# Optimization experiments

Measured on AMD Instinct MI355X. Metric: run time of the kernel, lower is better.

Reference implementation:

```python
import jax, jax.numpy as jnp
import numpy as np

B, IN_DIM, H1, H2, C = 8192, 1024, 2048, 2048, 1000
E, TOP_K, RH = 8, 2, 512
QB = 127.0
EPS = 1e-5


def _ste_round(x):
    # straight-through estimator round (BitNet-style)
    return x + jax.lax.stop_gradient(jnp.round(x) - x)


def _act_quant(x):
    # per-token absmax 8-bit activation quantization
    s = QB / jnp.clip(jnp.max(jnp.abs(x), axis=-1, keepdims=True), EPS, None)
    return jnp.clip(_ste_round(x * s), -QB, QB) / s


def _weight_quant(w):
    # ternary 1.58b weight quantization, per-tensor mean-abs scale
    s = jnp.clip(jnp.mean(jnp.abs(w)), EPS, None)
    return jnp.clip(_ste_round(w / s), -1.0, 1.0) * s


def _bit_linear(x, w, b):
    return _act_quant(x) @ _weight_quant(w).T + b


def setup_inputs() -> dict:
    key = jax.random.key(0)
    ks = jax.random.split(key, 12)
    def init(k, shape, fan_in):
        return (jax.random.normal(k, shape, dtype=jnp.float32) / np.sqrt(fan_in)).astype(jnp.float32)
    return {
        "x":  jax.random.normal(ks[0], (B, IN_DIM), dtype=jnp.float32),
        "Wr1": init(ks[1], (RH, IN_DIM), IN_DIM),
        "br1": jnp.zeros((RH,), jnp.float32),
        "Wr2": init(ks[2], (E, RH), RH),
        "br2": jnp.zeros((E,), jnp.float32),
        "W1": init(ks[3], (E, H1, IN_DIM), IN_DIM),
        "b1": jnp.zeros((E, H1), jnp.float32),
        "W2": init(ks[4], (E, H2, H1), H1),
        "b2": jnp.zeros((E, H2), jnp.float32),
        "W3": init(ks[5], (E, C, H2), H2),
        "b3": jnp.zeros((E, C), jnp.float32),
    }


def _forward(x, Wr1, br1, Wr2, br2, W1, b1, W2, b2, W3, b3):
    # Router (eval mode: dropout off)
    h = jax.nn.relu(x @ Wr1.T + br1)
    router_probs = jax.nn.softmax(h @ Wr2.T + br2, axis=1)       # [B, E]
    topk_vals, topk_idx = jax.lax.top_k(router_probs, TOP_K)     # [B, K]

    # dense gate matrix: gate[b,e] = sum_k topk_vals[b,k] * (topk_idx[b,k]==e)
    gates = jnp.sum(topk_vals[..., None] * jax.nn.one_hot(topk_idx, E, dtype=x.dtype), axis=1)  # [B, E]

    def expert(w1, c1, w2, c2, w3, c3):
        y = jax.nn.relu(_bit_linear(x, w1, c1))
        y = jax.nn.relu(_bit_linear(y, w2, c2))
        return _bit_linear(y, w3, c3)                             # [B, C]

    out_all = jax.vmap(expert)(W1, b1, W2, b2, W3, b3)            # [E, B, C]
    outputs = jnp.einsum('ebc,be->bc', out_all, gates) / TOP_K    # [B, C]
    load_balancing_loss = jnp.zeros((), x.dtype)                  # eval mode
    return outputs, router_probs, load_balancing_loss


def reference(x, Wr1, br1, Wr2, br2, W1, b1, W2, b2, W3, b3):
    return _forward(x, Wr1, br1, Wr2, br2, W1, b1, W2, b2, W3, b3)
```

## Files before the change

### kernel.cpp

```cpp
#include <hip/hip_runtime.h>
#include <stdint.h>

#define DEV static __device__ __forceinline__

typedef int v4i __attribute__((ext_vector_type(4)));
typedef short v8s __attribute__((ext_vector_type(8)));
typedef float v4f __attribute__((ext_vector_type(4)));
typedef unsigned short u16x8 __attribute__((ext_vector_type(8)));

constexpr int B_T   = 8192;
constexpr int IN_D  = 1024;
constexpr int H1D   = 2048;
constexpr int H2D   = 2048;
constexpr int CDIM  = 1000;
constexpr int NEXP  = 8;
constexpr int RHD   = 512;
constexpr float QBF  = 127.0f;
constexpr float EPSF = 1e-5f;
constexpr int NSLOT = 2 * B_T;
constexpr int MAXT  = 72;
constexpr float GAP_DELTA = 2e-3f;

DEV void load_lds16(const void* g, void* l) {
  __builtin_amdgcn_global_load_lds(
      (const __attribute__((address_space(1))) uint32_t*)(uintptr_t)g,
      (__attribute__((address_space(3))) uint32_t*)(uint32_t)(uintptr_t)l,
      16, 0, 0);
}

DEV uint32_t pack4(float a, float b, float c, float d, float s) {
  int q0 = (int)rintf(a * s); q0 = q0 > 127 ? 127 : (q0 < -127 ? -127 : q0);
  int q1 = (int)rintf(b * s); q1 = q1 > 127 ? 127 : (q1 < -127 ? -127 : q1);
  int q2 = (int)rintf(c * s); q2 = q2 > 127 ? 127 : (q2 < -127 ? -127 : q2);
  int q3 = (int)rintf(d * s); q3 = q3 > 127 ? 127 : (q3 < -127 ? -127 : q3);
  return (uint32_t)(uint8_t)q0 | ((uint32_t)(uint8_t)q1 << 8) |
         ((uint32_t)(uint8_t)q2 << 16) | ((uint32_t)(uint8_t)q3 << 24);
}

DEV uint16_t f2bf(float f) {
  uint32_t u = __float_as_uint(f);
  return (uint16_t)((u + 0x7FFFu + ((u >> 16) & 1u)) >> 16);
}
DEV float bf2f(uint16_t h) { return __uint_as_float((uint32_t)h << 16); }

DEV const float* slice_base(int t, const float* W1, const float* W2, const float* W3,
                            long& n4) {
  const float* W; long perExpert;
  if (t < 8)       { W = W1; perExpert = (long)H1D * IN_D; }
  else if (t < 16) { W = W2; perExpert = (long)H2D * H1D; }
  else             { W = W3; perExpert = (long)CDIM * H2D; }
  n4 = perExpert >> 2;
  return W + (long)(t & 7) * perExpert;
}

__global__ __launch_bounds__(256) void wabs_all(const float* __restrict__ W1,
                                                const float* __restrict__ W2,
                                                const float* __restrict__ W3,
                                                double* __restrict__ partial) {
  const int t = blockIdx.y;
  long n4;
  const float4* base = (const float4*)slice_base(t, W1, W2, W3, n4);
  double s0 = 0.0, s1 = 0.0, s2 = 0.0, s3 = 0.0;
  const long stride4 = 64L * 256L * 4L;
  for (long i4 = ((long)blockIdx.x * 256 + threadIdx.x) * 4; i4 < n4; i4 += stride4) {
    float4 a = base[i4 + 0];
    float4 b = base[i4 + 1];
    float4 c = base[i4 + 2];
    float4 d = base[i4 + 3];
    s0 += (double)fabsf(a.x) + (double)fabsf(a.y) + (double)fabsf(a.z) + (double)fabsf(a.w);
    s1 += (double)fabsf(b.x) + (double)fabsf(b.y) + (double)fabsf(b.z) + (double)fabsf(b.w);
    s2 += (double)fabsf(c.x) + (double)fabsf(c.y) + (double)fabsf(c.z) + (double)fabsf(c.w);
    s3 += (double)fabsf(d.x) + (double)fabsf(d.y) + (double)fabsf(d.z) + (double)fabsf(d.w);
  }
  __shared__ double red[256];
  red[threadIdx.x] = (s0 + s1) + (s2 + s3);
  __syncthreads();
  for (int st = 128; st > 0; st >>= 1) {
    if ((int)threadIdx.x < st) red[threadIdx.x] += red[threadIdx.x + st];
    __syncthreads();
  }
  if (threadIdx.x == 0) partial[(long)t * 64 + blockIdx.x] = red[0];
}

__global__ void finalize_scales(const double* __restrict__ partial, float* __restrict__ swf) {
  int t = threadIdx.x;
  if (t >= 24) return;
  double s = 0.0;
  for (int i = 0; i < 64; ++i) s += partial[t * 64 + i];
  long cnt = (t < 8) ? (long)H1D * IN_D : (t < 16) ? (long)H2D * H1D : (long)CDIM * H2D;
  float mean = (float)(s / (double)cnt);
  swf[t] = fmaxf(mean, EPSF);
}

__global__ __launch_bounds__(256) void wquant_all(const float* __restrict__ W1,
                                                  const float* __restrict__ W2,
                                                  const float* __restrict__ W3,
                                                  int8_t* __restrict__ wq1,
                                                  int8_t* __restrict__ wq2,
                                                  int8_t* __restrict__ wq3,
                                                  const float* __restrict__ swf) {
  const int t = blockIdx.y;
  long n4;
  const float4* base = (const float4*)slice_base(t, W1, W2, W3, n4);
  int8_t* Wq = (t < 8) ? wq1 : (t < 16) ? wq2 : wq3;
  uint32_t* out = (uint32_t*)(Wq) + (long)(t & 7) * n4;
  const float s = swf[t];
  const long stride4 = 64L * 256L * 4L;
  for (long i4 = ((long)blockIdx.x * 256 + threadIdx.x) * 4; i4 < n4; i4 += stride4) {
#pragma unroll
    for (int j = 0; j < 4; ++j) {
      float4 v = base[i4 + j];
      float t0 = fminf(fmaxf(rintf(v.x / s), -1.f), 1.f);
      float t1 = fminf(fmaxf(rintf(v.y / s), -1.f), 1.f);
      float t2 = fminf(fmaxf(rintf(v.z / s), -1.f), 1.f);
      float t3 = fminf(fmaxf(rintf(v.w / s), -1.f), 1.f);
      out[i4 + j] = (uint32_t)(uint8_t)(int8_t)t0 | ((uint32_t)(uint8_t)(int8_t)t1 << 8) |
                    ((uint32_t)(uint8_t)(int8_t)t2 << 16) | ((uint32_t)(uint8_t)(int8_t)t3 << 24);
    }
  }
}

__global__ __launch_bounds__(256) void actquant_split(const float* __restrict__ X,
                                                      int8_t* __restrict__ Xq,
                                                      float* __restrict__ rcp_out,
                                                      uint16_t* __restrict__ xh,
                                                      uint16_t* __restrict__ xl) {
  const int row = blockIdx.x;
  const int tid = threadIdx.x;
  float4 v = ((const float4*)(X + (size_t)row * IN_D))[tid];
  float mx = fmaxf(fmaxf(fabsf(v.x), fabsf(v.y)), fmaxf(fabsf(v.z), fabsf(v.w)));
#pragma unroll
  for (int m = 1; m < 64; m <<= 1) mx = fmaxf(mx, __shfl_xor(mx, m));
  __shared__ float wmax[4];
  const int lane = tid & 63, w = tid >> 6;
  if (lane == 0) wmax[w] = mx;
  __syncthreads();
  mx = fmaxf(fmaxf(wmax[0], wmax[1]), fmaxf(wmax[2], wmax[3]));
  const float M = fmaxf(mx, EPSF);
  const float s = QBF / M;
  ((uint32_t*)(Xq + (size_t)row * IN_D))[tid] = pack4(v.x, v.y, v.z, v.w, s);
  if (tid == 0) rcp_out[row] = M / QBF;
  float f[4] = {v.x, v.y, v.z, v.w};
  ushort4 hh, ll;
  uint16_t h4[4], l4[4];
#pragma unroll
  for (int j = 0; j < 4; ++j) {
    h4[j] = f2bf(f[j]);
    l4[j] = f2bf(f[j] - bf2f(h4[j]));
  }
  hh.x = h4[0]; hh.y = h4[1]; hh.z = h4[2]; hh.w = h4[3];
  ll.x = l4[0]; ll.y = l4[1]; ll.z = l4[2]; ll.w = l4[3];
  ((ushort4*)xh)[(size_t)row * 256 + tid] = hh;
  ((ushort4*)xl)[(size_t)row * 256 + tid] = ll;
}

__global__ __launch_bounds__(256) void split_bf16(const float* __restrict__ src,
                                                  uint16_t* __restrict__ hi,
                                                  uint16_t* __restrict__ lo, long n4) {
  long i = (long)blockIdx.x * 256 + threadIdx.x;
  if (i >= n4) return;
  float4 v = ((const float4*)src)[i];
  float f[4] = {v.x, v.y, v.z, v.w};
  ushort4 hh, ll;
  uint16_t h4[4], l4[4];
#pragma unroll
  for (int j = 0; j < 4; ++j) {
    h4[j] = f2bf(f[j]);
    l4[j] = f2bf(f[j] - bf2f(h4[j]));
  }
  hh.x = h4[0]; hh.y = h4[1]; hh.z = h4[2]; hh.w = h4[3];
  ll.x = l4[0]; ll.y = l4[1]; ll.z = l4[2]; ll.w = l4[3];
  ((ushort4*)hi)[i] = hh;
  ((ushort4*)lo)[i] = ll;
}

__global__ __launch_bounds__(256) void actquant_y(const uint16_t* __restrict__ Y,
                                                  int8_t* __restrict__ Xq,
                                                  float* __restrict__ rcp_out) {
  const int row = blockIdx.x;
  const int tid = threadIdx.x;
  u16x8 v = ((const u16x8*)(Y + (size_t)row * 2048))[tid];
  float f[8];
  float mx = 0.f;
#pragma unroll
  for (int j = 0; j < 8; ++j) {
    f[j] = bf2f(v[j]);
    mx = fmaxf(mx, fabsf(f[j]));
  }
#pragma unroll
  for (int m = 1; m < 64; m <<= 1) mx = fmaxf(mx, __shfl_xor(mx, m));
  __shared__ float wmax[4];
  const int lane = tid & 63, w = tid >> 6;
  if (lane == 0) wmax[w] = mx;
  __syncthreads();
  mx = fmaxf(fmaxf(wmax[0], wmax[1]), fmaxf(wmax[2], wmax[3]));
  const float M = fmaxf(mx, EPSF);
  const float s = QBF / M;
  uint2 o;
  o.x = pack4(f[0], f[1], f[2], f[3], s);
  o.y = pack4(f[4], f[5], f[6], f[7], s);
  ((uint2*)(Xq + (size_t)row * 2048))[tid] = o;
  if (tid == 0) rcp_out[row] = M / QBF;
}

__global__ __launch_bounds__(256, 1) void router_mfma(
    const uint16_t* __restrict__ xh, const uint16_t* __restrict__ xl,
    const uint16_t* __restrict__ wh, const uint16_t* __restrict__ wl,
    const float* __restrict__ br1, float* __restrict__ h) {
  __shared__ __align__(16) int8_t smem[2][65536];
  const int tid = threadIdx.x;
  const int lane = tid & 63, wid = tid >> 6;
  const int wm = wid >> 1, wn = wid & 1;
  const int row0 = blockIdx.x * 128, col0 = blockIdx.y * 128;

  const uint16_t* mats[4] = {xh, xl, wh, wl};
  const int rb[4] = {row0, row0, col0, col0};
  const uint8_t* src[16];
#pragma unroll
  for (int R = 0; R < 4; ++R)
#pragma unroll
    for (int i = 0; i < 4; ++i) {
      int p = i * 256 + tid;
      int r = p >> 3, c = p & 7;
      int cs = c ^ (r & 7);
      src[R * 4 + i] = (const uint8_t*)mats[R] + ((long)(rb[R] + r) * IN_D + cs * 8) * 2;
    }

  v4f acc[4][4] = {};
  auto stage = [&](int buf, int kt) {
#pragma unroll
    for (int R = 0; R < 4; ++R)
#pragma unroll
      for (int i = 0; i < 4; ++i)
        load_lds16(src[R * 4 + i] + kt * 128,
                   &smem[buf][R * 16384 + i * 4096 + wid * 1024]);
  };

  stage(0, 0);
  asm volatile("s_waitcnt vmcnt(0)" ::: "memory");
  __syncthreads();
  int buf = 0;
  for (int kt = 0; kt < 16; ++kt) {
    if (kt + 1 < 16) stage(buf ^ 1, kt + 1);
#pragma unroll
    for (int ks = 0; ks < 2; ++ks) {
      v8s ah[4], al[4], bh[4], bl[4];
#pragma unroll
      for (int m = 0; m < 4; ++m) {
        int r = wm * 64 + m * 16 + (lane & 15);
        int ch = (ks * 4 + (lane >> 4)) ^ (r & 7);
        ah[m] = *(const v8s*)&smem[buf][r * 128 + ch * 16];
        al[m] = *(const v8s*)&smem[buf][16384 + r * 128 + ch * 16];
      }
#pragma unroll
      for (int n = 0; n < 4; ++n) {
        int r = wn * 64 + n * 16 + (lane & 15);
        int ch = (ks * 4 + (lane >> 4)) ^ (r & 7);
        bh[n] = *(const v8s*)&smem[buf][32768 + r * 128 + ch * 16];
        bl[n] = *(const v8s*)&smem[buf][49152 + r * 128 + ch * 16];
      }
#pragma unroll
      for (int m = 0; m < 4; ++m)
#pragma unroll
        for (int n = 0; n < 4; ++n) {
          acc[m][n] = __builtin_amdgcn_mfma_f32_16x16x32_bf16(ah[m], bh[n], acc[m][n], 0, 0, 0);
          acc[m][n] = __builtin_amdgcn_mfma_f32_16x16x32_bf16(ah[m], bl[n], acc[m][n], 0, 0, 0);
          acc[m][n] = __builtin_amdgcn_mfma_f32_16x16x32_bf16(al[m], bh[n], acc[m][n], 0, 0, 0);
        }
    }
    asm volatile("s_waitcnt vmcnt(0)" ::: "memory");
    __syncthreads();
    buf ^= 1;
  }

  const int rbase = (lane >> 4) * 4;
  const int cfr = lane & 15;
#pragma unroll
  for (int m = 0; m < 4; ++m)
#pragma unroll
    for (int rg = 0; rg < 4; ++rg) {
      int row = row0 + wm * 64 + m * 16 + rbase + rg;
#pragma unroll
      for (int n = 0; n < 4; ++n) {
        int col = col0 + wn * 64 + n * 16 + cfr;
        h[(long)row * RHD + col] = fmaxf(acc[m][n][rg] + br1[col], 0.f);
      }
    }
}

__global__ __launch_bounds__(256) void router_stage2(const float* __restrict__ h,
                                                     const float* __restrict__ Wr2,
                                                     const float* __restrict__ br2,
                                                     float* __restrict__ probs,
                                                     int* __restrict__ idxg,
                                                     float* __restrict__ gvg,
                                                     int* __restrict__ scount,
                                                     int* __restrict__ suspects) {
  __shared__ float w2s[NEXP * RHD];
  const int tid = threadIdx.x;
  for (int i = tid; i < NEXP * RHD; i += 256) w2s[i] = Wr2[i];
  __syncthreads();
  const int lane = tid & 63, w = tid >> 6;
  const int b = blockIdx.x * 4 + w;
  const float* hrow = h + (long)b * RHD;
  float4 v0 = *(const float4*)&hrow[lane * 8];
  float4 v1 = *(const float4*)&hrow[lane * 8 + 4];
  float hr[8] = {v0.x, v0.y, v0.z, v0.w, v1.x, v1.y, v1.z, v1.w};
  float lg[8];
#pragma unroll
  for (int e = 0; e < 8; ++e) {
    float p = 0.f;
#pragma unroll
    for (int j = 0; j < 8; ++j) p = fmaf(hr[j], w2s[e * RHD + lane * 8 + j], p);
#pragma unroll
    for (int m = 1; m < 64; m <<= 1) p += __shfl_xor(p, m);
    lg[e] = p + br2[e];
  }
  if (lane == 0) {
    float mx = lg[0];
#pragma unroll
    for (int e = 1; e < 8; ++e) mx = fmaxf(mx, lg[e]);
    float ex[8], sum = 0.f;
#pragma unroll
    for (int e = 0; e < 8; ++e) { ex[e] = expf(lg[e] - mx); sum += ex[e]; }
#pragma unroll
    for (int e = 0; e < 8; ++e) probs[(long)b * 8 + e] = ex[e] / sum;
    int i0 = 0; float b0 = lg[0];
#pragma unroll
    for (int e = 1; e < 8; ++e) if (lg[e] > b0) { b0 = lg[e]; i0 = e; }
    int i1 = -1; float b1v = -3.4e38f;
#pragma unroll
    for (int e = 0; e < 8; ++e) if (e != i0 && lg[e] > b1v) { b1v = lg[e]; i1 = e; }
    float b2v = -3.4e38f;
#pragma unroll
    for (int e = 0; e < 8; ++e) if (e != i0 && e != i1 && lg[e] > b2v) b2v = lg[e];
    idxg[b * 2 + 0] = i0; idxg[b * 2 + 1] = i1;
    gvg[b * 2 + 0] = ex[i0] / sum; gvg[b * 2 + 1] = ex[i1] / sum;
    if (b1v - b2v < GAP_DELTA) {
      int p = atomicAdd(scount, 1);
      if (p < B_T) suspects[p] = b;
    }
  }
}

__global__ __launch_bounds__(256) void router_fixup(const float* __restrict__ x,
                                                    const float* __restrict__ Wr1,
                                                    const float* __restrict__ br1,
                                                    const float* __restrict__ Wr2,
                                                    const float* __restrict__ br2,
                                                    const int* __restrict__ suspects,
                                                    const int* __restrict__ scount,
                                                    float* __restrict__ probs,
                                                    int* __restrict__ idxg,
                                                    float* __restrict__ gvg) {
  __shared__ float xr[IN_D];
  __shared__ float hr[RHD];
  __shared__ float lgs[NEXP];
  const int n = *scount;
  const int tid = threadIdx.x;
  for (int s = blockIdx.x; s < n && s < B_T; s += 128) {
    const int b = suspects[s];
    __syncthreads();
    for (int i = tid; i < IN_D; i += 256) xr[i] = x[(long)b * IN_D + i];
    __syncthreads();
    {
      const int c0 = tid * 2, c1 = tid * 2 + 1;
      const float* w0 = Wr1 + (long)c0 * IN_D;
      const float* w1 = Wr1 + (long)c1 * IN_D;
      float a0 = 0.f, a1 = 0.f;
      for (int k = 0; k < IN_D; ++k) {
        float xv = xr[k];
        a0 = fmaf(xv, w0[k], a0);
        a1 = fmaf(xv, w1[k], a1);
      }
      hr[c0] = fmaxf(a0 + br1[c0], 0.f);
      hr[c1] = fmaxf(a1 + br1[c1], 0.f);
    }
    __syncthreads();
    if (tid < NEXP) {
      const float* w2 = Wr2 + (long)tid * RHD;
      float a = 0.f;
      for (int k = 0; k < RHD; ++k) a = fmaf(hr[k], w2[k], a);
      lgs[tid] = a + br2[tid];
    }
    __syncthreads();
    if (tid == 0) {
      float lg[8];
#pragma unroll
      for (int e = 0; e < 8; ++e) lg[e] = lgs[e];
      float mx = lg[0];
#pragma unroll
      for (int e = 1; e < 8; ++e) mx = fmaxf(mx, lg[e]);
      float ex[8], sum = 0.f;
#pragma unroll
      for (int e = 0; e < 8; ++e) { ex[e] = expf(lg[e] - mx); sum += ex[e]; }
#pragma unroll
      for (int e = 0; e < 8; ++e) probs[(long)b * 8 + e] = ex[e] / sum;
      int i0 = 0; float b0 = lg[0];
#pragma unroll
      for (int e = 1; e < 8; ++e) if (lg[e] > b0) { b0 = lg[e]; i0 = e; }
      int i1 = -1; float b1v = -3.4e38f;
#pragma unroll
      for (int e = 0; e < 8; ++e) if (e != i0 && lg[e] > b1v) { b1v = lg[e]; i1 = e; }
      idxg[b * 2 + 0] = i0; idxg[b * 2 + 1] = i1;
      gvg[b * 2 + 0] = ex[i0] / sum; gvg[b * 2 + 1] = ex[i1] / sum;
    }
  }
}

__global__ __launch_bounds__(256) void hist_block(const int* __restrict__ idxg,
                                                  int* __restrict__ bc) {
  __shared__ int hloc[NEXP];
  const int t = threadIdx.x;
  if (t < NEXP) hloc[t] = 0;
  __syncthreads();
  int a = blockIdx.x * 256 + t;
  atomicAdd(&hloc[idxg[a]], 1);
  __syncthreads();
  if (t < NEXP) bc[blockIdx.x * NEXP + t] = hloc[t];
}

__global__ void scan_all(const int* __restrict__ bc, int* __restrict__ blockbase,
                         int* __restrict__ ntiles, int* __restrict__ te,
                         int* __restrict__ ts, int* __restrict__ tc,
                         float* __restrict__ loss_out) {
  __shared__ int counts[NEXP], basep[NEXP];
  const int t = threadIdx.x;
  if (t < NEXP) {
    int s = 0;
    for (int b = 0; b < 64; ++b) s += bc[b * NEXP + t];
    counts[t] = s;
  }
  __syncthreads();
  if (t == 0) {
    int acc = 0, nb = 0;
    for (int e = 0; e < NEXP; ++e) {
      basep[e] = acc;
      int c = counts[e];
      int nt = (c + 255) >> 8;
      for (int i = 0; i < nt; ++i) {
        te[nb] = e; ts[nb] = acc + i * 256; tc[nb] = min(256, c - i * 256); ++nb;
      }
      acc += c;
    }
    *ntiles = nb;
    *loss_out = 0.f;
  }
  __syncthreads();
  if (t < NEXP) {
    int run = basep[t];
    for (int b = 0; b < 64; ++b) { blockbase[b * NEXP + t] = run; run += bc[b * NEXP + t]; }
  }
}

__global__ __launch_bounds__(256) void place2(const int* __restrict__ idxg,
                                              const int* __restrict__ blockbase,
                                              int* __restrict__ token_list,
                                              int* __restrict__ slotmap) {
  __shared__ int cur[NEXP];
  const int t = threadIdx.x;
  if (t < NEXP) cur[t] = blockbase[blockIdx.x * NEXP + t];
  __syncthreads();
  int a = blockIdx.x * 256 + t;
  int e = idxg[a];
  int pos = atomicAdd(&cur[e], 1);
  token_list[pos] = a >> 1;
  slotmap[a] = pos;
}

template <int KDIM, bool INDIRECT, bool RELU, bool FINAL>
__global__ __launch_bounds__(512, 2) void gemm_i8(
    const int8_t* __restrict__ Aq, const int8_t* __restrict__ Wq,
    const float* __restrict__ swf_layer, const float* __restrict__ rcp_act,
    const float* __restrict__ bias, const int* __restrict__ te,
    const int* __restrict__ ts, const int* __restrict__ tc,
    const int* __restrict__ ntiles_p, const int* __restrict__ token_list,
    void* __restrict__ Yout, int Nvalid) {
  if ((int)blockIdx.y >= *ntiles_p) return;
  extern __shared__ __align__(16) int8_t smem_dyn[];
  const int t = blockIdx.y;
  const int e = te[t], row0 = ts[t], rcount = tc[t];
  const int col0 = blockIdx.x * 256;
  const int tid = threadIdx.x;
  const int lane = tid & 63, wid = tid >> 6;
  const int wsm = wid >> 2, wsn = wid & 3;
  const int fr = lane & 15, hi = lane >> 4;

  const int8_t* sA[2][2];
  const int8_t* sB[2][2];
#pragma unroll
  for (int hh = 0; hh < 2; ++hh)
#pragma unroll
    for (int i = 0; i < 2; ++i) {
      int p = i * 512 + tid;
      int rl = p >> 3, c = p & 7;
      int cs = c ^ (rl & 7);
      int rt = hh * 128 + rl;
      int ar = row0 + min(rt, rcount - 1);
      long arow = INDIRECT ? (long)token_list[ar] : (long)ar;
      sA[hh][i] = Aq + arow * KDIM + cs * 16;
      int br = min(col0 + rt, Nvalid - 1);
      sB[hh][i] = Wq + ((long)e * Nvalid + br) * (long)KDIM + cs * 16;
    }

  auto stage = [&](int buf, int kt, int which) {
    const int hh = which & 1;
    const bool isB = which >= 2;
    const int8_t* p0 = isB ? sB[hh][0] : sA[hh][0];
    const int8_t* p1 = isB ? sB[hh][1] : sA[hh][1];
    int base = buf * 65536 + (isB ? 32768 : 0) + hh * 16384 + wid * 1024;
    load_lds16(p0 + (long)kt * 128, &smem_dyn[base]);
    load_lds16(p1 + (long)kt * 128, &smem_dyn[base + 8192]);
  };

  const int swz0 = ((0 * 4 + hi) ^ (fr & 7)) * 16 + fr * 128;
  const int swz1 = ((1 * 4 + hi) ^ (fr & 7)) * 16 + fr * 128;

  v4i acc[2][2][4][2] = {};
  v4i aF[4][2];
  v4i bF[2][2][2];

  constexpr int KT = KDIM / 128;
  stage(0, 0, 0); stage(0, 0, 1); stage(0, 0, 2); stage(0, 0, 3);
  stage(1, 1, 0); stage(1, 1, 2); stage(1, 1, 1);
  asm volatile("s_waitcnt vmcnt(6)" ::: "memory");
  asm volatile("s_barrier" ::: "memory");

  for (int kt = 0; kt < KT; ++kt) {
    const int buf = kt & 1;
    const int ab = buf * 65536;
    const int bb = ab + 32768;
#pragma unroll
    for (int mi = 0; mi < 4; ++mi) {
      aF[mi][0] = *(const v4i*)&smem_dyn[ab + (wsm * 64 + mi * 16) * 128 + swz0];
      aF[mi][1] = *(const v4i*)&smem_dyn[ab + (wsm * 64 + mi * 16) * 128 + swz1];
    }
#pragma unroll
    for (int ni = 0; ni < 2; ++ni) {
      bF[0][ni][0] = *(const v4i*)&smem_dyn[bb + (wsn * 32 + ni * 16) * 128 + swz0];
      bF[0][ni][1] = *(const v4i*)&smem_dyn[bb + (wsn * 32 + ni * 16) * 128 + swz1];
    }
    if (kt + 1 < KT) stage(buf ^ 1, kt + 1, 3);
    __builtin_amdgcn_s_setprio(1);
#pragma unroll
    for (int mi = 0; mi < 4; ++mi)
#pragma unroll
      for (int ni = 0; ni < 2; ++ni) {
        acc[0][0][mi][ni] = __builtin_amdgcn_mfma_i32_16x16x64_i8(aF[mi][0], bF[0][ni][0], acc[0][0][mi][ni], 0, 0, 0);
        acc[0][0][mi][ni] = __builtin_amdgcn_mfma_i32_16x16x64_i8(aF[mi][1], bF[0][ni][1], acc[0][0][mi][ni], 0, 0, 0);
      }
    __builtin_amdgcn_s_setprio(0);
    asm volatile("s_barrier" ::: "memory");
#pragma unroll
    for (int ni = 0; ni < 2; ++ni) {
      bF[1][ni][0] = *(const v4i*)&smem_dyn[bb + (128 + wsn * 32 + ni * 16) * 128 + swz0];
      bF[1][ni][1] = *(const v4i*)&smem_dyn[bb + (128 + wsn * 32 + ni * 16) * 128 + swz1];
    }
    if (kt + 2 < KT) stage(buf, kt + 2, 0);
    __builtin_amdgcn_s_setprio(1);
#pragma unroll
    for (int mi = 0; mi < 4; ++mi)
#pragma unroll
      for (int ni = 0; ni < 2; ++ni) {
        acc[0][1][mi][ni] = __builtin_amdgcn_mfma_i32_16x16x64_i8(aF[mi][0], bF[1][ni][0], acc[0][1][mi][ni], 0, 0, 0);
        acc[0][1][mi][ni] = __builtin_amdgcn_mfma_i32_16x16x64_i8(aF[mi][1], bF[1][ni][1], acc[0][1][mi][ni], 0, 0, 0);
      }
    __builtin_amdgcn_s_setprio(0);
    asm volatile("s_barrier" ::: "memory");
#pragma unroll
    for (int mi = 0; mi < 4; ++mi) {
      aF[mi][0] = *(const v4i*)&smem_dyn[ab + (128 + wsm * 64 + mi * 16) * 128 + swz0];
      aF[mi][1] = *(const v4i*)&smem_dyn[ab + (128 + wsm * 64 + mi * 16) * 128 + swz1];
    }
    if (kt + 2 < KT) stage(buf, kt + 2, 2);
    __builtin_amdgcn_s_setprio(1);
#pragma unroll
    for (int mi = 0; mi < 4; ++mi)
#pragma unroll
      for (int ni = 0; ni < 2; ++ni) {
        acc[1][0][mi][ni] = __builtin_amdgcn_mfma_i32_16x16x64_i8(aF[mi][0], bF[0][ni][0], acc[1][0][mi][ni], 0, 0, 0);
        acc[1][0][mi][ni] = __builtin_amdgcn_mfma_i32_16x16x64_i8(aF[mi][1], bF[0][ni][1], acc[1][0][mi][ni], 0, 0, 0);
      }
    __builtin_amdgcn_s_setprio(0);
    asm volatile("s_barrier" ::: "memory");
    if (kt + 2 < KT) stage(buf, kt + 2, 1);
    __builtin_amdgcn_s_setprio(1);
#pragma unroll
    for (int mi = 0; mi < 4; ++mi)
#pragma unroll
      for (int ni = 0; ni < 2; ++ni) {
        acc[1][1][mi][ni] = __builtin_amdgcn_mfma_i32_16x16x64_i8(aF[mi][0], bF[1][ni][0], acc[1][1][mi][ni], 0, 0, 0);
        acc[1][1][mi][ni] = __builtin_amdgcn_mfma_i32_16x16x64_i8(aF[mi][1], bF[1][ni][1], acc[1][1][mi][ni], 0, 0, 0);
      }
    __builtin_amdgcn_s_setprio(0);
    if (kt < KT - 3) {
      asm volatile("s_waitcnt vmcnt(6)" ::: "memory");
    } else {
      asm volatile("s_waitcnt vmcnt(0)" ::: "memory");
    }
    asm volatile("s_barrier" ::: "memory");
  }

  const float sw = swf_layer[e];
  const int rbase = hi * 4;
  const float* bias_e = bias + (long)e * Nvalid;
#pragma unroll
  for (int qm = 0; qm < 2; ++qm)
#pragma unroll
    for (int mi = 0; mi < 4; ++mi)
#pragma unroll
      for (int rg = 0; rg < 4; ++rg) {
        int trow = qm * 128 + wsm * 64 + mi * 16 + rbase + rg;
        if (trow >= rcount) continue;
        int slot = row0 + trow;
        float rcp = rcp_act[INDIRECT ? token_list[slot] : slot];
        float dq = sw * rcp;
        if constexpr (!FINAL) {
          uint16_t* yrow = (uint16_t*)Yout + (long)slot * 2048;
#pragma unroll
          for (int qn = 0; qn < 2; ++qn)
#pragma unroll
            for (int ni = 0; ni < 2; ++ni) {
              int o = col0 + qn * 128 + wsn * 32 + ni * 16 + fr;
              float v = (float)acc[qm][qn][mi][ni][rg] * dq + bias_e[o];
              if (RELU) v = fmaxf(v, 0.f);
              yrow[o] = f2bf(v);
            }
        } else {
          float* zrow = (float*)Yout + (long)slot * 1024;
#pragma unroll
          for (int qn = 0; qn < 2; ++qn)
#pragma unroll
            for (int ni = 0; ni < 2; ++ni) {
              int o = col0 + qn * 128 + wsn * 32 + ni * 16 + fr;
              float bb2 = bias_e[min(o, Nvalid - 1)];
              zrow[o] = (float)acc[qm][qn][mi][ni][rg] * dq + bb2;
            }
        }
      }
}

__global__ __launch_bounds__(256) void combine(const float* __restrict__ z,
                                               const int* __restrict__ slotmap,
                                               const float* __restrict__ gvg,
                                               float* __restrict__ out) {
  const int b = blockIdx.x;
  const int c = threadIdx.x;
  if (c >= 250) return;
  const int s0 = slotmap[b * 2], s1 = slotmap[b * 2 + 1];
  const float g0 = gvg[b * 2] * 0.5f, g1 = gvg[b * 2 + 1] * 0.5f;
  float4 a = *(const float4*)(z + (long)s0 * 1024 + c * 4);
  float4 q = *(const float4*)(z + (long)s1 * 1024 + c * 4);
  float4 o = {g0 * a.x + g1 * q.x, g0 * a.y + g1 * q.y,
              g0 * a.z + g1 * q.z, g0 * a.w + g1 * q.w};
  *(float4*)(out + (long)b * CDIM + c * 4) = o;
}

extern "C" void kernel_launch(void* const* d_in, const int* in_sizes, int n_in,
                              void* d_out, int out_size, void* d_ws, size_t ws_size,
                              hipStream_t stream) {
  const float* x   = (const float*)d_in[0];
  const float* Wr1 = (const float*)d_in[1];
  const float* br1 = (const float*)d_in[2];
  const float* Wr2 = (const float*)d_in[3];
  const float* br2 = (const float*)d_in[4];
  const float* W1  = (const float*)d_in[5];
  const float* b1  = (const float*)d_in[6];
  const float* W2  = (const float*)d_in[7];
  const float* b2  = (const float*)d_in[8];
  const float* W3  = (const float*)d_in[9];
  const float* b3  = (const float*)d_in[10];
  float* out = (float*)d_out;
  char* ws = (char*)d_ws;

  size_t off = 0;
  auto alloc = [&](size_t sz) { size_t r = off; off = (off + sz + 255) & ~(size_t)255; return r; };
  size_t O_META  = alloc(8192);
  size_t O_SUSP  = alloc(B_T * sizeof(int));
  size_t O_PART  = alloc(24 * 64 * sizeof(double));
  size_t O_SWF   = alloc(24 * sizeof(float));
  size_t O_RCPX  = alloc(B_T * sizeof(float));
  size_t O_IDX   = alloc(B_T * 2 * sizeof(int));
  size_t O_GVG   = alloc(B_T * 2 * sizeof(float));
  size_t O_TLIST = alloc(NSLOT * sizeof(int));
  size_t O_SLOT  = alloc(B_T * 2 * sizeof(int));
  size_t O_S1    = alloc(NSLOT * sizeof(float));
  size_t O_S2    = alloc(NSLOT * sizeof(float));
  size_t O_XQ    = alloc((size_t)B_T * IN_D);
  size_t O_WQ1   = alloc((size_t)NEXP * H1D * IN_D);
  size_t O_WQ2   = alloc((size_t)NEXP * H2D * H1D);
  size_t O_WQ3   = alloc((size_t)NEXP * CDIM * H2D);
  size_t O_YQ    = alloc((size_t)NSLOT * 2048);
  size_t O_YBIG  = alloc((size_t)NSLOT * 2048 * sizeof(float));
  (void)ws_size; (void)in_sizes; (void)n_in;

  int*    te     = (int*)(ws + O_META);
  int*    tsv    = te + 144;
  int*    tcv    = tsv + 144;
  int*    ntiles = tcv + 144;
  int*    bc     = ntiles + 4;
  int*    bbase  = bc + 512;
  int*    scount = bbase + 512;
  int*    susp   = (int*)(ws + O_SUSP);
  double* part   = (double*)(ws + O_PART);
  float*  swf    = (float*)(ws + O_SWF);
  float*  rcpx   = (float*)(ws + O_RCPX);
  int*    idxg   = (int*)(ws + O_IDX);
  float*  gvg    = (float*)(ws + O_GVG);
  int*    tlist  = (int*)(ws + O_TLIST);
  int*    slotmap= (int*)(ws + O_SLOT);
  float*  s1     = (float*)(ws + O_S1);
  float*  s2     = (float*)(ws + O_S2);
  int8_t* Xq     = (int8_t*)(ws + O_XQ);
  int8_t* wq1    = (int8_t*)(ws + O_WQ1);
  int8_t* wq2    = (int8_t*)(ws + O_WQ2);
  int8_t* wq3    = (int8_t*)(ws + O_WQ3);
  float*  Ybig   = (float*)(ws + O_YBIG);
  float*  h      = Ybig;
  uint16_t* ybf  = (uint16_t*)Ybig;
  float*  zbuf   = Ybig;
  int8_t* Yq     = (int8_t*)(ws + O_YQ);

  char* ybytes = (char*)Ybig;
  uint16_t* xh = (uint16_t*)(ybytes + (80l << 20));
  uint16_t* xl = (uint16_t*)(ybytes + (97l << 20));
  uint16_t* wh = (uint16_t*)(ybytes + (114l << 20));
  uint16_t* wl = (uint16_t*)(ybytes + (116l << 20));

  hipMemsetAsync(ws + O_META, 0, 8192, stream);

  wabs_all<<<dim3(64, 24), 256, 0, stream>>>(W1, W2, W3, part);
  finalize_scales<<<1, 64, 0, stream>>>(part, swf);
  wquant_all<<<dim3(64, 24), 256, 0, stream>>>(W1, W2, W3, wq1, wq2, wq3, swf);

  actquant_split<<<B_T, 256, 0, stream>>>(x, Xq, rcpx, xh, xl);
  split_bf16<<<512, 256, 0, stream>>>(Wr1, wh, wl, (long)RHD * IN_D / 4);

  router_mfma<<<dim3(B_T / 128, RHD / 128), 256, 0, stream>>>(xh, xl, wh, wl, br1, h);
  router_stage2<<<B_T / 4, 256, 0, stream>>>(h, Wr2, br2, out + (size_t)B_T * CDIM,
                                             idxg, gvg, scount, susp);
  router_fixup<<<128, 256, 0, stream>>>(x, Wr1, br1, Wr2, br2, susp, scount,
                                        out + (size_t)B_T * CDIM, idxg, gvg);
  hist_block<<<64, 256, 0, stream>>>(idxg, bc);
  scan_all<<<1, 64, 0, stream>>>(bc, bbase, ntiles, te, tsv, tcv,
                                 out + (size_t)B_T * CDIM + (size_t)B_T * NEXP);
  place2<<<64, 256, 0, stream>>>(idxg, bbase, tlist, slotmap);

  gemm_i8<IN_D, true, true, false><<<dim3(H1D / 256, MAXT), 512, 131072, stream>>>(
      Xq, wq1, swf + 0, rcpx, b1, te, tsv, tcv, ntiles, tlist, (void*)ybf, H1D);
  actquant_y<<<NSLOT, 256, 0, stream>>>(ybf, Yq, s1);
  gemm_i8<2048, false, true, false><<<dim3(H2D / 256, MAXT), 512, 131072, stream>>>(
      Yq, wq2, swf + 8, s1, b2, te, tsv, tcv, ntiles, tlist, (void*)ybf, H2D);
  actquant_y<<<NSLOT, 256, 0, stream>>>(ybf, Yq, s2);
  gemm_i8<2048, false, false, true><<<dim3(1024 / 256, MAXT), 512, 131072, stream>>>(
      Yq, wq3, swf + 16, s2, b3, te, tsv, tcv, ntiles, tlist, (void*)zbuf, CDIM);

  combine<<<B_T, 256, 0, stream>>>(zbuf, slotmap, gvg, out);
}
```

Measured before the change: 565.8 us.

## Halve GEMM K-tile to 64 and restructure pipeline for higher occupancy

The int8 MFMA GEMM now uses a K step of 64 instead of 128, with a new swizzle and a single 16-byte load per thread per stage. This halves LDS use to 64KB per block and raises launch bounds to allow 4 blocks per CU, aiming to hide latency through occupancy. The prefetch schedule changes from loading two K tiles ahead to one tile ahead, with mid-iteration waits. The cost is twice as many iterations and barriers per unit of K and a shallower prefetch, and the tighter register budget may cause spills.

```diff
diff --git a/kernel.cpp b/kernel.cpp
--- a/kernel.cpp
+++ b/kernel.cpp
@@ -469,7 +469,7 @@
 }
 
 template <int KDIM, bool INDIRECT, bool RELU, bool FINAL>
-__global__ __launch_bounds__(512, 2) void gemm_i8(
+__global__ __launch_bounds__(512, 4) void gemm_i8(
     const int8_t* __restrict__ Aq, const int8_t* __restrict__ Wq,
     const float* __restrict__ swf_layer, const float* __restrict__ rcp_act,
     const float* __restrict__ bias, const int* __restrict__ te,
@@ -486,119 +486,95 @@
   const int wsm = wid >> 2, wsn = wid & 3;
   const int fr = lane & 15, hi = lane >> 4;
 
-  const int8_t* sA[2][2];
-  const int8_t* sB[2][2];
-#pragma unroll
-  for (int hh = 0; hh < 2; ++hh)
-#pragma unroll
-    for (int i = 0; i < 2; ++i) {
-      int p = i * 512 + tid;
-      int rl = p >> 3, c = p & 7;
-      int cs = c ^ (rl & 7);
-      int rt = hh * 128 + rl;
+  const int8_t* sA[2];
+  const int8_t* sB[2];
+  {
+    int r = tid >> 2, c = tid & 3;
+    int cs = c ^ ((r >> 1) & 3);
+#pragma unroll
+    for (int hh = 0; hh < 2; ++hh) {
+      int rt = hh * 128 + r;
       int ar = row0 + min(rt, rcount - 1);
       long arow = INDIRECT ? (long)token_list[ar] : (long)ar;
-      sA[hh][i] = Aq + arow * KDIM + cs * 16;
+      sA[hh] = Aq + arow * KDIM + cs * 16;
       int br = min(col0 + rt, Nvalid - 1);
-      sB[hh][i] = Wq + ((long)e * Nvalid + br) * (long)KDIM + cs * 16;
-    }
+      sB[hh] = Wq + ((long)e * Nvalid + br) * (long)KDIM + cs * 16;
+    }
+  }
 
   auto stage = [&](int buf, int kt, int which) {
     const int hh = which & 1;
-    const bool isB = which >= 2;
-    const int8_t* p0 = isB ? sB[hh][0] : sA[hh][0];
-    const int8_t* p1 = isB ? sB[hh][1] : sA[hh][1];
-    int base = buf * 65536 + (isB ? 32768 : 0) + hh * 16384 + wid * 1024;
-    load_lds16(p0 + (long)kt * 128, &smem_dyn[base]);
-    load_lds16(p1 + (long)kt * 128, &smem_dyn[base + 8192]);
+    const int8_t* p = (which >= 2) ? sB[hh] : sA[hh];
+    int dst = buf * 32768 + (which & 1) * 8192 + ((which >> 1) & 1) * 16384 + wid * 1024;
+    load_lds16(p + (long)kt * 64, &smem_dyn[dst]);
   };
 
-  const int swz0 = ((0 * 4 + hi) ^ (fr & 7)) * 16 + fr * 128;
-  const int swz1 = ((1 * 4 + hi) ^ (fr & 7)) * 16 + fr * 128;
+  const int swzc = (hi ^ ((fr >> 1) & 3)) * 16 + fr * 64;
 
   v4i acc[2][2][4][2] = {};
-  v4i aF[4][2];
-  v4i bF[2][2][2];
-
-  constexpr int KT = KDIM / 128;
-  stage(0, 0, 0); stage(0, 0, 1); stage(0, 0, 2); stage(0, 0, 3);
-  stage(1, 1, 0); stage(1, 1, 2); stage(1, 1, 1);
-  asm volatile("s_waitcnt vmcnt(6)" ::: "memory");
-  asm volatile("s_barrier" ::: "memory");
+  v4i aF[4];
+  v4i bF[2][2];
+
+  constexpr int KT = KDIM / 64;
+  stage(0, 0, 3); stage(0, 0, 0); stage(0, 0, 2); stage(0, 0, 1);
 
   for (int kt = 0; kt < KT; ++kt) {
     const int buf = kt & 1;
-    const int ab = buf * 65536;
-    const int bb = ab + 32768;
-#pragma unroll
-    for (int mi = 0; mi < 4; ++mi) {
-      aF[mi][0] = *(const v4i*)&smem_dyn[ab + (wsm * 64 + mi * 16) * 128 + swz0];
-      aF[mi][1] = *(const v4i*)&smem_dyn[ab + (wsm * 64 + mi * 16) * 128 + swz1];
-    }
-#pragma unroll
-    for (int ni = 0; ni < 2; ++ni) {
-      bF[0][ni][0] = *(const v4i*)&smem_dyn[bb + (wsn * 32 + ni * 16) * 128 + swz0];
-      bF[0][ni][1] = *(const v4i*)&smem_dyn[bb + (wsn * 32 + ni * 16) * 128 + swz1];
-    }
+    const int base = buf * 32768;
+    asm volatile("s_waitcnt vmcnt(1)" ::: "memory");
+    asm volatile("s_barrier" ::: "memory");
+#pragma unroll
+    for (int mi = 0; mi < 4; ++mi)
+      aF[mi] = *(const v4i*)&smem_dyn[base + (wsm * 64 + mi * 16) * 64 + swzc];
+#pragma unroll
+    for (int ni = 0; ni < 2; ++ni)
+      bF[0][ni] = *(const v4i*)&smem_dyn[base + 16384 + (wsn * 32 + ni * 16) * 64 + swzc];
     if (kt + 1 < KT) stage(buf ^ 1, kt + 1, 3);
     __builtin_amdgcn_s_setprio(1);
 #pragma unroll
     for (int mi = 0; mi < 4; ++mi)
 #pragma unroll
-      for (int ni = 0; ni < 2; ++ni) {
-        acc[0][0][mi][ni] = __builtin_amdgcn_mfma_i32_16x16x64_i8(aF[mi][0], bF[0][ni][0], acc[0][0][mi][ni], 0, 0, 0);
-        acc[0][0][mi][ni] = __builtin_amdgcn_mfma_i32_16x16x64_i8(aF[mi][1], bF[0][ni][1], acc[0][0][mi][ni], 0, 0, 0);
-      }
+      for (int ni = 0; ni < 2; ++ni)
+        acc[0][0][mi][ni] = __builtin_amdgcn_mfma_i32_16x16x64_i8(aF[mi], bF[0][ni], acc[0][0][mi][ni], 0, 0, 0);
     __builtin_amdgcn_s_setprio(0);
     asm volatile("s_barrier" ::: "memory");
 #pragma unroll
-    for (int ni = 0; ni < 2; ++ni) {
-      bF[1][ni][0] = *(const v4i*)&smem_dyn[bb + (128 + wsn * 32 + ni * 16) * 128 + swz0];
-      bF[1][ni][1] = *(const v4i*)&smem_dyn[bb + (128 + wsn * 32 + ni * 16) * 128 + swz1];
-    }
-    if (kt + 2 < KT) stage(buf, kt + 2, 0);
+    for (int ni = 0; ni < 2; ++ni)
+      bF[1][ni] = *(const v4i*)&smem_dyn[base + 24576 + (wsn * 32 + ni * 16) * 64 + swzc];
+    if (kt + 1 < KT) stage(buf ^ 1, kt + 1, 0);
     __builtin_amdgcn_s_setprio(1);
 #pragma unroll
     for (int mi = 0; mi < 4; ++mi)
 #pragma unroll
-      for (int ni = 0; ni < 2; ++ni) {
-        acc[0][1][mi][ni] = __builtin_amdgcn_mfma_i32_16x16x64_i8(aF[mi][0], bF[1][ni][0], acc[0][1][mi][ni], 0, 0, 0);
-        acc[0][1][mi][ni] = __builtin_amdgcn_mfma_i32_16x16x64_i8(aF[mi][1], bF[1][ni][1], acc[0][1][mi][ni], 0, 0, 0);
-      }
+      for (int ni = 0; ni < 2; ++ni)
+        acc[0][1][mi][ni] = __builtin_amdgcn_mfma_i32_16x16x64_i8(aF[mi], bF[1][ni], acc[0][1][mi][ni], 0, 0, 0);
+    __builtin_amdgcn_s_setprio(0);
+    if (kt + 1 < KT) {
+      asm volatile("s_waitcnt vmcnt(2)" ::: "memory");
+    } else {
+      asm volatile("s_waitcnt vmcnt(0)" ::: "memory");
+    }
+    asm volatile("s_barrier" ::: "memory");
+#pragma unroll
+    for (int mi = 0; mi < 4; ++mi)
+      aF[mi] = *(const v4i*)&smem_dyn[base + 8192 + (wsm * 64 + mi * 16) * 64 + swzc];
+    if (kt + 1 < KT) stage(buf ^ 1, kt + 1, 2);
+    __builtin_amdgcn_s_setprio(1);
+#pragma unroll
+    for (int mi = 0; mi < 4; ++mi)
+#pragma unroll
+      for (int ni = 0; ni < 2; ++ni)
+        acc[1][0][mi][ni] = __builtin_amdgcn_mfma_i32_16x16x64_i8(aF[mi], bF[0][ni], acc[1][0][mi][ni], 0, 0, 0);
     __builtin_amdgcn_s_setprio(0);
     asm volatile("s_barrier" ::: "memory");
-#pragma unroll
-    for (int mi = 0; mi < 4; ++mi) {
-      aF[mi][0] = *(const v4i*)&smem_dyn[ab + (128 + wsm * 64 + mi * 16) * 128 + swz0];
-      aF[mi][1] = *(const v4i*)&smem_dyn[ab + (128 + wsm * 64 + mi * 16) * 128 + swz1];
-    }
-    if (kt + 2 < KT) stage(buf, kt + 2, 2);
+    if (kt + 1 < KT) stage(buf ^ 1, kt + 1, 1);
     __builtin_amdgcn_s_setprio(1);
 #pragma unroll
     for (int mi = 0; mi < 4; ++mi)
 #pragma unroll
-      for (int ni = 0; ni < 2; ++ni) {
-        acc[1][0][mi][ni] = __builtin_amdgcn_mfma_i32_16x16x64_i8(aF[mi][0], bF[0][ni][0], acc[1][0][mi][ni], 0, 0, 0);
-        acc[1][0][mi][ni] = __builtin_amdgcn_mfma_i32_16x16x64_i8(aF[mi][1], bF[0][ni][1], acc[1][0][mi][ni], 0, 0, 0);
-      }
+      for (int ni = 0; ni < 2; ++ni)
+        acc[1][1][mi][ni] = __builtin_amdgcn_mfma_i32_16x16x64_i8(aF[mi], bF[1][ni], acc[1][1][mi][ni], 0, 0, 0);
     __builtin_amdgcn_s_setprio(0);
-    asm volatile("s_barrier" ::: "memory");
-    if (kt + 2 < KT) stage(buf, kt + 2, 1);
-    __builtin_amdgcn_s_setprio(1);
-#pragma unroll
-    for (int mi = 0; mi < 4; ++mi)
-#pragma unroll
-      for (int ni = 0; ni < 2; ++ni) {
-        acc[1][1][mi][ni] = __builtin_amdgcn_mfma_i32_16x16x64_i8(aF[mi][0], bF[1][ni][0], acc[1][1][mi][ni], 0, 0, 0);
-        acc[1][1][mi][ni] = __builtin_amdgcn_mfma_i32_16x16x64_i8(aF[mi][1], bF[1][ni][1], acc[1][1][mi][ni], 0, 0, 0);
-      }
-    __builtin_amdgcn_s_setprio(0);
-    if (kt < KT - 3) {
-      asm volatile("s_waitcnt vmcnt(6)" ::: "memory");
-    } else {
-      asm volatile("s_waitcnt vmcnt(0)" ::: "memory");
-    }
-    asm volatile("s_barrier" ::: "memory");
   }
 
   const float sw = swf_layer[e];
@@ -746,13 +722,13 @@
                                  out + (size_t)B_T * CDIM + (size_t)B_T * NEXP);
   place2<<<64, 256, 0, stream>>>(idxg, bbase, tlist, slotmap);
 
-  gemm_i8<IN_D, true, true, false><<<dim3(H1D / 256, MAXT), 512, 131072, stream>>>(
+  gemm_i8<IN_D, true, true, false><<<dim3(H1D / 256, MAXT), 512, 65536, stream>>>(
       Xq, wq1, swf + 0, rcpx, b1, te, tsv, tcv, ntiles, tlist, (void*)ybf, H1D);
   actquant_y<<<NSLOT, 256, 0, stream>>>(ybf, Yq, s1);
-  gemm_i8<2048, false, true, false><<<dim3(H2D / 256, MAXT), 512, 131072, stream>>>(
+  gemm_i8<2048, false, true, false><<<dim3(H2D / 256, MAXT), 512, 65536, stream>>>(
       Yq, wq2, swf + 8, s1, b2, te, tsv, tcv, ntiles, tlist, (void*)ybf, H2D);
   actquant_y<<<NSLOT, 256, 0, stream>>>(ybf, Yq, s2);
-  gemm_i8<2048, false, false, true><<<dim3(1024 / 256, MAXT), 512, 131072, stream>>>(
+  gemm_i8<2048, false, false, true><<<dim3(1024 / 256, MAXT), 512, 65536, stream>>>(
       Yq, wq3, swf + 16, s2, b3, te, tsv, tcv, ntiles, tlist, (void*)zbuf, CDIM);
 
   combine<<<B_T, 256, 0, stream>>>(zbuf, slotmap, gvg, out);
```

Result: slower. 1.798 ms (+217.7%).
